# Kernel tuning notes

Hardware: AMD Instinct MI355X
Metric: run time of the kernel (lower is better)

## Reference

```python
import jax, jax.numpy as jnp
import numpy as np

B, N, C, H = 16, 1024, 768, 12
D = C // H          # head dim = 64
HID = 4 * C         # 3072
EPS = 1e-5


def layernorm(x, g, b):
    m = x.mean(-1, keepdims=True)
    v = ((x - m) ** 2).mean(-1, keepdims=True)
    return (x - m) * jax.lax.rsqrt(v + EPS) * g + b


def setup_inputs() -> dict:
    key = jax.random.key(0)
    ks = jax.random.split(key, 10)
    s = 0.02
    return {
        "x": jax.random.normal(ks[0], (B, N, C), dtype=jnp.float32),
        "ln1_g": jnp.ones((C,), jnp.float32), "ln1_b": jnp.zeros((C,), jnp.float32),
        "wq": jax.random.normal(ks[1], (C, C)) * s, "bq": jnp.zeros((C,), jnp.float32),
        "wk": jax.random.normal(ks[2], (C, C)) * s, "bk": jnp.zeros((C,), jnp.float32),
        "wv": jax.random.normal(ks[3], (C, C)) * s, "bv": jnp.zeros((C,), jnp.float32),
        "wp": jax.random.normal(ks[4], (C, C)) * s, "bp": jnp.zeros((C,), jnp.float32),
        "ln2_g": jnp.ones((C,), jnp.float32), "ln2_b": jnp.zeros((C,), jnp.float32),
        "w1": jax.random.normal(ks[5], (HID, C)) * s, "b1": jnp.zeros((HID,), jnp.float32),
        "w2": jax.random.normal(ks[6], (C, HID)) * s, "b2": jnp.zeros((C,), jnp.float32),
        "gate_h": jax.random.normal(ks[7], (H,), dtype=jnp.float32),
        "gate_f": jax.random.normal(ks[8], (HID,), dtype=jnp.float32),
    }


def reference(x, ln1_g, ln1_b, wq, bq, wk, bk, wv, bv, wp, bp,
              ln2_g, ln2_b, w1, b1, w2, b2, gate_h, gate_f):
    # steady-state path: k_dynamic=None, is_warmup=False -> dyn gates are all ones,
    # so head_mask / ffn_mask reduce to the hard static gates (STE is identity on ones).
    head_mask = (jax.nn.sigmoid(gate_h) > 0.5).astype(x.dtype)            # [H]
    hm = jnp.broadcast_to(head_mask, (B, H))                              # [B,H]

    # --- attention branch ---
    xn = layernorm(x, ln1_g, ln1_b)
    split = lambda t: t.reshape(B, N, H, D).transpose(0, 2, 1, 3)          # [B,H,N,D]
    q = split(xn @ wq.T + bq)
    k = split(xn @ wk.T + bk)
    v = split(xn @ wv.T + bv)
    scale = D ** -0.5
    attn = jax.nn.softmax(jnp.einsum('bhqd,bhkd->bhqk', q, k) * scale, axis=-1)
    y = jnp.einsum('bhqk,bhkd->bhqd', attn, v)
    y = y * hm[:, :, None, None]                                           # per-head mask on y
    xa = y.transpose(0, 2, 1, 3).reshape(B, N, C)
    hm_flat = jnp.repeat(hm, D, axis=-1).reshape(B, 1, C)                  # mask applied a 2nd time
    xa = (xa * hm_flat) @ wp.T + bp
    x = x + xa

    # --- gated MLP branch ---
    fmask = (jax.nn.sigmoid(gate_f) > 0.5).astype(x.dtype)[None, None, :]  # [1,1,HID]
    xn2 = layernorm(x, ln2_g, ln2_b)
    f1 = xn2 @ w1.T + b1
    f1 = jax.nn.gelu(f1 * fmask, approximate=False) * fmask                # mask -> GELU -> mask
    x = x + f1 @ w2.T + b2
    return x
```

## Files before the change

### kernel.cpp

```cpp
#include <hip/hip_runtime.h>

#define BB 16
#define NNN 1024
#define CC 768
#define HH 12
#define DD 64
#define HIDN 3072
#define ROWS (BB*NNN)

typedef _Float16 half8 __attribute__((ext_vector_type(8)));
typedef _Float16 half4 __attribute__((ext_vector_type(4)));
typedef float floatx4 __attribute__((ext_vector_type(4)));

#define GLOAD_LDS(g, l) __builtin_amdgcn_global_load_lds( \
    (const __attribute__((address_space(1))) void*)(g),    \
    (__attribute__((address_space(3))) void*)(l), 16, 0, 0)

#define RAW_BARRIER() do { asm volatile("" ::: "memory"); \
    __builtin_amdgcn_s_barrier(); asm volatile("" ::: "memory"); } while (0)
#define VMCNT_WAIT(n) __builtin_amdgcn_s_waitcnt((n) | 0x0F70)

__global__ void cvt_kernel(const float* __restrict__ src, _Float16* __restrict__ dst, int n4) {
    int i = blockIdx.x * blockDim.x + threadIdx.x;
    if (i < n4) {
        floatx4 v = ((const floatx4*)src)[i];
        half4 h;
        h[0] = (_Float16)v[0]; h[1] = (_Float16)v[1];
        h[2] = (_Float16)v[2]; h[3] = (_Float16)v[3];
        ((half4*)dst)[i] = h;
    }
}

__global__ __launch_bounds__(256) void scan_kernel(const float* __restrict__ gf,
                                                   const float* __restrict__ b1,
                                                   int* __restrict__ meta,
                                                   int* __restrict__ perm,
                                                   float* __restrict__ b1c) {
    int t = threadIdx.x;
    int base = t * 12;
    bool act[12];
    int cnt = 0;
    #pragma unroll
    for (int i = 0; i < 12; i++) { bool a = gf[base + i] > 0.0f; act[i] = a; cnt += a ? 1 : 0; }
    __shared__ int cs[256];
    __shared__ int tot;
    cs[t] = cnt;
    __syncthreads();
    if (t == 0) {
        int s = 0;
        for (int i = 0; i < 256; i++) { int c = cs[i]; cs[i] = s; s += c; }
        tot = s;
        meta[1] = s;
        meta[0] = (s + 127) & ~127;
    }
    __syncthreads();
    int off = cs[t];
    for (int i = t; i < HIDN; i += 256) { b1c[i] = 0.0f; perm[i] = -1; }
    __syncthreads();
    #pragma unroll
    for (int i = 0; i < 12; i++)
        if (act[i]) { perm[off] = base + i; b1c[off] = b1[base + i]; off++; }
    (void)tot;
}

__global__ void gatherW1_kernel(const float* __restrict__ src, const int* __restrict__ perm,
                                _Float16* __restrict__ dst) {
    int i = blockIdx.x * blockDim.x + threadIdx.x;
    int row = i / 192, c4 = i - row * 192;
    int s = perm[row];
    half4 h; h[0] = h[1] = h[2] = h[3] = (_Float16)0.0f;
    if (s >= 0) {
        floatx4 v = ((const floatx4*)(src + (size_t)s * CC))[c4];
        h[0] = (_Float16)v[0]; h[1] = (_Float16)v[1];
        h[2] = (_Float16)v[2]; h[3] = (_Float16)v[3];
    }
    ((half4*)dst)[i] = h;
}

__global__ void gatherW2_kernel(const float* __restrict__ src, const int* __restrict__ perm,
                                _Float16* __restrict__ dst) {
    int i = blockIdx.x * blockDim.x + threadIdx.x;
    int n = i / 768, j4 = (i - n * 768) * 4;
    const float* r = src + (size_t)n * HIDN;
    half4 h;
    #pragma unroll
    for (int e = 0; e < 4; e++) {
        int s = perm[j4 + e];
        h[e] = (s >= 0) ? (_Float16)r[s] : (_Float16)0.0f;
    }
    *(half4*)&dst[(size_t)n * HIDN + j4] = h;
}

__global__ __launch_bounds__(256) void ln_kernel(const float* __restrict__ x,
                                                 const float* __restrict__ g,
                                                 const float* __restrict__ b,
                                                 _Float16* __restrict__ out) {
    int row = blockIdx.x;
    int t = threadIdx.x;
    const float* xr = x + (size_t)row * CC;
    float v0 = xr[t], v1 = xr[t + 256], v2 = xr[t + 512];
    float s = v0 + v1 + v2;
    float q = v0 * v0 + v1 * v1 + v2 * v2;
    #pragma unroll
    for (int m = 1; m < 64; m <<= 1) {
        s += __shfl_xor(s, m, 64);
        q += __shfl_xor(q, m, 64);
    }
    __shared__ float red[8];
    int wv = t >> 6, lane = t & 63;
    if (lane == 0) { red[wv] = s; red[wv + 4] = q; }
    __syncthreads();
    s = red[0] + red[1] + red[2] + red[3];
    q = red[4] + red[5] + red[6] + red[7];
    float mean = s * (1.0f / CC);
    float var = q * (1.0f / CC) - mean * mean;
    float rs = rsqrtf(var + 1e-5f);
    _Float16* orow = out + (size_t)row * CC;
    orow[t]       = (_Float16)((v0 - mean) * rs * g[t]       + b[t]);
    orow[t + 256] = (_Float16)((v1 - mean) * rs * g[t + 256] + b[t + 256]);
    orow[t + 512] = (_Float16)((v2 - mean) * rs * g[t + 512] + b[t + 512]);
}

template <int MODE, int TM>
__global__ __launch_bounds__(256) void gemm_kernel(
    const _Float16* __restrict__ A,
    const _Float16* __restrict__ W,
    const float* __restrict__ bias0,
    const float* __restrict__ bias1,
    const float* __restrict__ bias2,
    const float* __restrict__ res,
    const float* __restrict__ gate,
    const float* __restrict__ hgate,
    void* __restrict__ out0,
    void* __restrict__ out1,
    void* __restrict__ out2,
    const int* __restrict__ meta,
    int M, int N, int K)
{
    constexpr int MI = TM / 32;
    constexpr int AISS = TM / 64;
    constexpr int NISS = AISS + 2;
    int GN = N >> 7, GM = M / TM;
    int f = blockIdx.x;
    int xcd = f & 7, slot = f >> 3;
    int m_idx = xcd * (GM >> 3) + slot / GN;
    int n_idx = slot - (slot / GN) * GN;
    int m0 = m_idx * TM, n0 = n_idx * 128;

    int Klen = K;
    if (meta) {
        if (MODE == 1) { if (n0 >= meta[0]) return; }
        if (MODE == 2) Klen = meta[0];
    }

    int seg = 0;
    if (MODE == 0) {
        seg = n0 / 768;
        int segc0 = n0 - seg * 768;
        int h0 = segc0 >> 6;
        if (hgate[h0] <= 0.0f && hgate[h0 + 1] <= 0.0f) return;
    }
    unsigned kmask = 0xFFFFFFFFu;
    if (MODE == 2 && hgate) {
        kmask = 0;
        for (int i = 0; i < HH; i++) kmask |= (hgate[i] > 0.0f ? 1u : 0u) << i;
    }

    __shared__ _Float16 As[3][TM * 32];
    __shared__ _Float16 Bs[3][128 * 32];
    int t = threadIdx.x;
    int lane = t & 63, w = t >> 6;
    int wm = (w >> 1) * (TM / 2), wn = (w & 1) * 64;
    int L = lane & 15, quad = lane >> 4;
    int rchunk = (quad ^ ((L >> 2) & 3)) * 8;

    floatx4 acc[MI][4];
    #pragma unroll
    for (int i = 0; i < MI; i++)
        #pragma unroll
        for (int j = 0; j < 4; j++)
            acc[i][j] = (floatx4){0.f, 0.f, 0.f, 0.f};

    const _Float16* agp[AISS];
    const _Float16* bgp[2];
    #pragma unroll
    for (int i = 0; i < AISS; i++) {
        int pc = i * 256 + t;
        int row = pc >> 2;
        int kc = (pc & 3) ^ ((pc >> 4) & 3);
        agp[i] = A + (size_t)(m0 + row) * K + kc * 8;
    }
    #pragma unroll
    for (int i = 0; i < 2; i++) {
        int pc = i * 256 + t;
        int row = pc >> 2;
        int kc = (pc & 3) ^ ((pc >> 4) & 3);
        bgp[i] = W + (size_t)(n0 + row) * K + kc * 8;
    }
    unsigned wb = (unsigned)w * 512;

    auto nextk = [&](int k0) -> int {
        if (MODE == 2)
            while (k0 < Klen && !((kmask >> ((k0 >> 6) & 31)) & 1)) k0 += 32;
        return k0;
    };
    auto stage = [&](int buf, int k0) {
        #pragma unroll
        for (int i = 0; i < AISS; i++) GLOAD_LDS(agp[i] + k0, &As[buf][i * 2048 + wb]);
        #pragma unroll
        for (int i = 0; i < 2; i++)    GLOAD_LDS(bgp[i] + k0, &Bs[buf][i * 2048 + wb]);
    };
    auto compute = [&](int buf) {
        half8 af[MI], bf[4];
        #pragma unroll
        for (int i = 0; i < MI; i++) af[i] = *(const half8*)&As[buf][(wm + i * 16 + L) * 32 + rchunk];
        #pragma unroll
        for (int j = 0; j < 4; j++)  bf[j] = *(const half8*)&Bs[buf][(wn + j * 16 + L) * 32 + rchunk];
        #pragma unroll
        for (int i = 0; i < MI; i++)
            #pragma unroll
            for (int j = 0; j < 4; j++)
                acc[i][j] = __builtin_amdgcn_mfma_f32_16x16x32_f16(af[i], bf[j], acc[i][j], 0, 0, 0);
    };

    int kcur = nextk(0);
    if (kcur < Klen) {
        stage(0, kcur);
        int kn1 = nextk(kcur + 32);
        int kn2 = Klen;
        if (kn1 < Klen) { stage(1, kn1); kn2 = nextk(kn1 + 32); }
        int buf = 0;
        while (kn2 < Klen) {
            int bnext = buf + 2; if (bnext >= 3) bnext -= 3;
            stage(bnext, kn2);
            VMCNT_WAIT(2 * NISS);
            RAW_BARRIER();
            compute(buf);
            RAW_BARRIER();
            buf = buf + 1; if (buf >= 3) buf -= 3;
            kcur = kn1; kn1 = kn2; kn2 = nextk(kn2 + 32);
        }
        if (kn1 < Klen) {
            VMCNT_WAIT(NISS);
            RAW_BARRIER();
            compute(buf);
            buf = buf + 1; if (buf >= 3) buf -= 3;
        }
        VMCNT_WAIT(0);
        RAW_BARRIER();
        compute(buf);
    }

    #pragma unroll
    for (int i = 0; i < MI; i++) {
        #pragma unroll
        for (int j = 0; j < 4; j++) {
            int gn = n0 + wn + j * 16 + L;
            if (MODE == 0) {
                int col = gn - seg * 768;
                const float* bsel = (seg == 0) ? bias0 : (seg == 1) ? bias1 : bias2;
                float bs = bsel[col];
                if (seg < 2) {
                    _Float16* o = (_Float16*)((seg == 0) ? out0 : out1);
                    #pragma unroll
                    for (int r = 0; r < 4; r++) {
                        int gm = m0 + wm + i * 16 + quad * 4 + r;
                        o[(size_t)gm * CC + col] = (_Float16)(acc[i][j][r] + bs);
                    }
                } else {
                    int gm0 = m0 + wm + i * 16 + quad * 4;
                    int b_ = gm0 >> 10, n_ = gm0 & 1023;
                    half4 pk;
                    #pragma unroll
                    for (int r = 0; r < 4; r++) pk[r] = (_Float16)(acc[i][j][r] + bs);
                    size_t idx = ((size_t)(b_ * HH + (col >> 6)) * 64 + (col & 63)) * NNN + n_;
                    *(half4*)&((_Float16*)out2)[idx] = pk;
                }
            } else {
                float bs = bias0[gn];
                #pragma unroll
                for (int r = 0; r < 4; r++) {
                    int gm = m0 + wm + i * 16 + quad * 4 + r;
                    float v = acc[i][j][r] + bs;
                    size_t idx = (size_t)gm * N + gn;
                    if (MODE == 1) {
                        float vv = 0.5f * v * (1.0f + erff(v * 0.70710678118f));
                        if (gate && !(gate[gn] > 0.0f)) vv = 0.0f;
                        ((_Float16*)out0)[idx] = (_Float16)vv;
                    } else {
                        ((float*)out0)[idx] = res[idx] + v;
                    }
                }
            }
        }
    }
}

__global__ __launch_bounds__(256) void attn_kernel(
    const _Float16* __restrict__ Q,
    const _Float16* __restrict__ Kp,
    const _Float16* __restrict__ Vt,
    const float* __restrict__ gate_h,
    _Float16* __restrict__ Y)
{
    int qt = blockIdx.x;
    int h  = blockIdx.y;
    int b  = blockIdx.z;
    int t = threadIdx.x;
    int q0 = qt * 64;
    size_t ybase = ((size_t)b * NNN + q0) * CC + h * DD;

    if (gate_h[h] <= 0.0f) {
        int r = t >> 2, c = (t & 3) * 16;
        half8 z = {(_Float16)0, (_Float16)0, (_Float16)0, (_Float16)0,
                   (_Float16)0, (_Float16)0, (_Float16)0, (_Float16)0};
        *(half8*)&Y[ybase + (size_t)r * CC + c]     = z;
        *(half8*)&Y[ybase + (size_t)r * CC + c + 8] = z;
        return;
    }

    __shared__ _Float16 Qs[64][72];
    __shared__ _Float16 Ks[64][72];
    __shared__ _Float16 Vs[64][72];
    __shared__ _Float16 Ps[64][72];

    int lane = t & 63, w = t >> 6;
    int L = lane & 15, quad = lane >> 4;

    {
        int r = t >> 2, c = (t & 3) * 16;
        const half8* src = (const half8*)(Q + ((size_t)b * NNN + q0 + r) * CC + h * DD + c);
        half8 h0 = src[0], h1 = src[1];
        #pragma unroll
        for (int e = 0; e < 8; e++) { h0[e] = h0[e] * (_Float16)0.125f; h1[e] = h1[e] * (_Float16)0.125f; }
        *(half8*)&Qs[r][c]     = h0;
        *(half8*)&Qs[r][c + 8] = h1;
    }

    floatx4 O[4];
    float m_[4], l_[4];
    #pragma unroll
    for (int i = 0; i < 4; i++) { O[i] = (floatx4){0.f,0.f,0.f,0.f}; m_[i] = -1e30f; l_[i] = 0.0f; }

    const size_t kbase = (size_t)b * NNN * CC + h * DD;
    const size_t vbase = (size_t)(b * HH + h) * DD * NNN;

    for (int kt = 0; kt < 16; ++kt) {
        int k0 = kt * 64;
        __syncthreads();
        {
            int r = t >> 2, c = (t & 3) * 16;
            const half8* ks = (const half8*)(Kp + kbase + (size_t)(k0 + r) * CC + c);
            half8 ka = ks[0], kb = ks[1];
            *(half8*)&Ks[r][c]     = ka;
            *(half8*)&Ks[r][c + 8] = kb;
            const half8* vs = (const half8*)(Vt + vbase + (size_t)r * NNN + k0 + c);
            half8 va = vs[0], vb = vs[1];
            *(half8*)&Vs[r][c]     = va;
            *(half8*)&Vs[r][c + 8] = vb;
        }
        __syncthreads();

        half8 aq0 = *(const half8*)&Qs[16 * w + L][quad * 8];
        half8 aq1 = *(const half8*)&Qs[16 * w + L][quad * 8 + 32];
        floatx4 s[4];
        #pragma unroll
        for (int j = 0; j < 4; j++) {
            half8 b0 = *(const half8*)&Ks[16 * j + L][quad * 8];
            half8 b1 = *(const half8*)&Ks[16 * j + L][quad * 8 + 32];
            floatx4 z = (floatx4){0.f,0.f,0.f,0.f};
            z = __builtin_amdgcn_mfma_f32_16x16x32_f16(aq0, b0, z, 0, 0, 0);
            z = __builtin_amdgcn_mfma_f32_16x16x32_f16(aq1, b1, z, 0, 0, 0);
            s[j] = z;
        }

        #pragma unroll
        for (int r = 0; r < 4; r++) {
            float mx = fmaxf(fmaxf(s[0][r], s[1][r]), fmaxf(s[2][r], s[3][r]));
            mx = fmaxf(mx, __shfl_xor(mx, 1, 64));
            mx = fmaxf(mx, __shfl_xor(mx, 2, 64));
            mx = fmaxf(mx, __shfl_xor(mx, 4, 64));
            mx = fmaxf(mx, __shfl_xor(mx, 8, 64));
            float mnew = fmaxf(m_[r], mx);
            float alpha = __expf(m_[r] - mnew);
            m_[r] = mnew;
            float ps = 0.0f;
            #pragma unroll
            for (int j = 0; j < 4; j++) {
                float p = __expf(s[j][r] - mnew);
                s[j][r] = p; ps += p;
                Ps[16 * w + quad * 4 + r][L + 16 * j] = (_Float16)p;
            }
            ps += __shfl_xor(ps, 1, 64);
            ps += __shfl_xor(ps, 2, 64);
            ps += __shfl_xor(ps, 4, 64);
            ps += __shfl_xor(ps, 8, 64);
            l_[r] = l_[r] * alpha + ps;
            #pragma unroll
            for (int t4 = 0; t4 < 4; t4++) O[t4][r] *= alpha;
        }
        __syncthreads();

        half8 ap0 = *(const half8*)&Ps[16 * w + L][quad * 8];
        half8 ap1 = *(const half8*)&Ps[16 * w + L][quad * 8 + 32];
        #pragma unroll
        for (int t4 = 0; t4 < 4; t4++) {
            half8 b0 = *(const half8*)&Vs[16 * t4 + L][quad * 8];
            half8 b1 = *(const half8*)&Vs[16 * t4 + L][quad * 8 + 32];
            O[t4] = __builtin_amdgcn_mfma_f32_16x16x32_f16(ap0, b0, O[t4], 0, 0, 0);
            O[t4] = __builtin_amdgcn_mfma_f32_16x16x32_f16(ap1, b1, O[t4], 0, 0, 0);
        }
    }

    __syncthreads();
    #pragma unroll
    for (int r = 0; r < 4; r++) {
        float inv = 1.0f / l_[r];
        #pragma unroll
        for (int t4 = 0; t4 < 4; t4++)
            Ps[16 * w + quad * 4 + r][16 * t4 + L] = (_Float16)(O[t4][r] * inv);
    }
    __syncthreads();
    {
        int r = t >> 2, c = (t & 3) * 16;
        half8 o0 = *(const half8*)&Ps[r][c];
        half8 o1 = *(const half8*)&Ps[r][c + 8];
        *(half8*)&Y[ybase + (size_t)r * CC + c]     = o0;
        *(half8*)&Y[ybase + (size_t)r * CC + c + 8] = o1;
    }
}

extern "C" void kernel_launch(void* const* d_in, const int* in_sizes, int n_in,
                              void* d_out, int out_size, void* d_ws, size_t ws_size,
                              hipStream_t stream)
{
    const float* x      = (const float*)d_in[0];
    const float* ln1_g  = (const float*)d_in[1];
    const float* ln1_b  = (const float*)d_in[2];
    const float* wq     = (const float*)d_in[3];
    const float* bq     = (const float*)d_in[4];
    const float* wk     = (const float*)d_in[5];
    const float* bk     = (const float*)d_in[6];
    const float* wv     = (const float*)d_in[7];
    const float* bv     = (const float*)d_in[8];
    const float* wp     = (const float*)d_in[9];
    const float* bp     = (const float*)d_in[10];
    const float* ln2_g  = (const float*)d_in[11];
    const float* ln2_b  = (const float*)d_in[12];
    const float* w1     = (const float*)d_in[13];
    const float* b1     = (const float*)d_in[14];
    const float* w2     = (const float*)d_in[15];
    const float* b2     = (const float*)d_in[16];
    const float* gate_h = (const float*)d_in[17];
    const float* gate_f = (const float*)d_in[18];

    char* ws = (char*)d_ws;
    _Float16* WQKVh = (_Float16*)(ws + 0);
    _Float16* WPh = (_Float16*)(ws + 3538944);
    _Float16* W1c = (_Float16*)(ws + 4718592);
    _Float16* W2c = (_Float16*)(ws + 9437184);
    _Float16* XN  = (_Float16*)(ws + 14155776);
    _Float16* Qb  = (_Float16*)(ws + 39321600);
    _Float16* Kb  = (_Float16*)(ws + 64487424);
    _Float16* Vtb = (_Float16*)(ws + 89653248);
    _Float16* Yb  = (_Float16*)(ws + 114819072);
    float*    X1  = (float*)   (ws + 139984896);
    _Float16* XN2 = (_Float16*)(ws + 114819072);
    _Float16* F1  = (_Float16*)(ws + 14155776);
    int*      meta = (int*)    (ws + 190316544);
    int*      perm = (int*)    (ws + 190316800);
    float*    b1c  = (float*)  (ws + 190329088);

    scan_kernel<<<1, 256, 0, stream>>>(gate_f, b1, meta, perm, b1c);

    cvt_kernel<<<576, 256, 0, stream>>>(wq, WQKVh, 147456);
    cvt_kernel<<<576, 256, 0, stream>>>(wk, WQKVh + 589824, 147456);
    cvt_kernel<<<576, 256, 0, stream>>>(wv, WQKVh + 1179648, 147456);
    cvt_kernel<<<576, 256, 0, stream>>>(wp, WPh, 147456);
    gatherW1_kernel<<<2304, 256, 0, stream>>>(w1, perm, W1c);
    gatherW2_kernel<<<2304, 256, 0, stream>>>(w2, perm, W2c);

    ln_kernel<<<ROWS, 256, 0, stream>>>(x, ln1_g, ln1_b, XN);

    gemm_kernel<0, 128><<<2304, 256, 0, stream>>>(
        XN, WQKVh, bq, bk, bv, nullptr, nullptr, gate_h, Qb, Kb, Vtb, nullptr, ROWS, 2304, CC);

    attn_kernel<<<dim3(16, HH, BB), 256, 0, stream>>>(Qb, Kb, Vtb, gate_h, Yb);

    gemm_kernel<2, 64><<<1536, 256, 0, stream>>>(
        Yb, WPh, bp, nullptr, nullptr, x, nullptr, gate_h, X1, nullptr, nullptr, nullptr, ROWS, CC, CC);

    ln_kernel<<<ROWS, 256, 0, stream>>>(X1, ln2_g, ln2_b, XN2);

    gemm_kernel<1, 128><<<3072, 256, 0, stream>>>(
        XN2, W1c, b1c, nullptr, nullptr, nullptr, nullptr, nullptr, F1, nullptr, nullptr, meta, ROWS, HIDN, CC);

    gemm_kernel<2, 128><<<768, 256, 0, stream>>>(
        F1, W2c, b2, nullptr, nullptr, X1, nullptr, nullptr, (float*)d_out, nullptr, nullptr, meta, ROWS, CC, HIDN);
}
```

Before: 515.8 us.

## Switch GEMM to BK=64 double-buffered pipeline with 8-chunk XOR swizzle

The GEMM kernel's K tile grows from 32 to 64, and the LDS pipeline drops from a triple buffer to a double buffer. LDS uses a new 8-way XOR swizzle, and each compute step runs two MFMA sub-steps. The next tile is staged only after the current one has been computed, which halves the barrier count per K but gives less load/compute overlap. The W2 GEMM also moves to TM=64 with twice the blocks, so more workgroups run on the long-K GEMM.

```diff
diff --git a/kernel.cpp b/kernel.cpp
--- a/kernel.cpp
+++ b/kernel.cpp
@@ -43,13 +43,11 @@
     #pragma unroll
     for (int i = 0; i < 12; i++) { bool a = gf[base + i] > 0.0f; act[i] = a; cnt += a ? 1 : 0; }
     __shared__ int cs[256];
-    __shared__ int tot;
     cs[t] = cnt;
     __syncthreads();
     if (t == 0) {
         int s = 0;
         for (int i = 0; i < 256; i++) { int c = cs[i]; cs[i] = s; s += c; }
-        tot = s;
         meta[1] = s;
         meta[0] = (s + 127) & ~127;
     }
@@ -60,7 +58,6 @@
     #pragma unroll
     for (int i = 0; i < 12; i++)
         if (act[i]) { perm[off] = base + i; b1c[off] = b1[base + i]; off++; }
-    (void)tot;
 }
 
 __global__ void gatherW1_kernel(const float* __restrict__ src, const int* __restrict__ perm,
@@ -138,8 +135,9 @@
     int M, int N, int K)
 {
     constexpr int MI = TM / 32;
-    constexpr int AISS = TM / 64;
-    constexpr int NISS = AISS + 2;
+    constexpr int AISS = TM / 32;
+    constexpr int BISS = 4;
+    constexpr int NISS = AISS + BISS;
     int GN = N >> 7, GM = M / TM;
     int f = blockIdx.x;
     int xcd = f & 7, slot = f >> 3;
@@ -166,13 +164,12 @@
         for (int i = 0; i < HH; i++) kmask |= (hgate[i] > 0.0f ? 1u : 0u) << i;
     }
 
-    __shared__ _Float16 As[3][TM * 32];
-    __shared__ _Float16 Bs[3][128 * 32];
+    __shared__ _Float16 As[2][TM * 64];
+    __shared__ _Float16 Bs[2][128 * 64];
     int t = threadIdx.x;
     int lane = t & 63, w = t >> 6;
     int wm = (w >> 1) * (TM / 2), wn = (w & 1) * 64;
     int L = lane & 15, quad = lane >> 4;
-    int rchunk = (quad ^ ((L >> 2) & 3)) * 8;
 
     floatx4 acc[MI][4];
     #pragma unroll
@@ -182,69 +179,73 @@
             acc[i][j] = (floatx4){0.f, 0.f, 0.f, 0.f};
 
     const _Float16* agp[AISS];
-    const _Float16* bgp[2];
+    const _Float16* bgp[BISS];
     #pragma unroll
     for (int i = 0; i < AISS; i++) {
         int pc = i * 256 + t;
-        int row = pc >> 2;
-        int kc = (pc & 3) ^ ((pc >> 4) & 3);
+        int row = pc >> 3;
+        int kc = (pc & 7) ^ (row & 7);
         agp[i] = A + (size_t)(m0 + row) * K + kc * 8;
     }
     #pragma unroll
-    for (int i = 0; i < 2; i++) {
+    for (int i = 0; i < BISS; i++) {
         int pc = i * 256 + t;
-        int row = pc >> 2;
-        int kc = (pc & 3) ^ ((pc >> 4) & 3);
+        int row = pc >> 3;
+        int kc = (pc & 7) ^ (row & 7);
         bgp[i] = W + (size_t)(n0 + row) * K + kc * 8;
     }
     unsigned wb = (unsigned)w * 512;
 
     auto nextk = [&](int k0) -> int {
         if (MODE == 2)
-            while (k0 < Klen && !((kmask >> ((k0 >> 6) & 31)) & 1)) k0 += 32;
+            while (k0 < Klen && !((kmask >> ((k0 >> 6) & 31)) & 1)) k0 += 64;
         return k0;
     };
     auto stage = [&](int buf, int k0) {
         #pragma unroll
         for (int i = 0; i < AISS; i++) GLOAD_LDS(agp[i] + k0, &As[buf][i * 2048 + wb]);
         #pragma unroll
-        for (int i = 0; i < 2; i++)    GLOAD_LDS(bgp[i] + k0, &Bs[buf][i * 2048 + wb]);
+        for (int i = 0; i < BISS; i++) GLOAD_LDS(bgp[i] + k0, &Bs[buf][i * 2048 + wb]);
     };
     auto compute = [&](int buf) {
-        half8 af[MI], bf[4];
-        #pragma unroll
-        for (int i = 0; i < MI; i++) af[i] = *(const half8*)&As[buf][(wm + i * 16 + L) * 32 + rchunk];
-        #pragma unroll
-        for (int j = 0; j < 4; j++)  bf[j] = *(const half8*)&Bs[buf][(wn + j * 16 + L) * 32 + rchunk];
-        #pragma unroll
-        for (int i = 0; i < MI; i++)
+        #pragma unroll
+        for (int kk = 0; kk < 2; kk++) {
+            half8 af[MI], bf[4];
+            #pragma unroll
+            for (int i = 0; i < MI; i++)
+                af[i] = *(const half8*)&As[buf][(wm + i * 16 + L) * 64 + ((kk * 4 + quad) ^ (L & 7)) * 8];
             #pragma unroll
             for (int j = 0; j < 4; j++)
-                acc[i][j] = __builtin_amdgcn_mfma_f32_16x16x32_f16(af[i], bf[j], acc[i][j], 0, 0, 0);
+                bf[j] = *(const half8*)&Bs[buf][(wn + j * 16 + L) * 64 + ((kk * 4 + quad) ^ (L & 7)) * 8];
+            #pragma unroll
+            for (int i = 0; i < MI; i++)
+                #pragma unroll
+                for (int j = 0; j < 4; j++)
+                    acc[i][j] = __builtin_amdgcn_mfma_f32_16x16x32_f16(af[i], bf[j], acc[i][j], 0, 0, 0);
+        }
     };
 
     int kcur = nextk(0);
     if (kcur < Klen) {
         stage(0, kcur);
-        int kn1 = nextk(kcur + 32);
+        int kn1 = nextk(kcur + 64);
         int kn2 = Klen;
-        if (kn1 < Klen) { stage(1, kn1); kn2 = nextk(kn1 + 32); }
+        if (kn1 < Klen) { stage(1, kn1); kn2 = nextk(kn1 + 64); }
         int buf = 0;
         while (kn2 < Klen) {
-            int bnext = buf + 2; if (bnext >= 3) bnext -= 3;
-            stage(bnext, kn2);
-            VMCNT_WAIT(2 * NISS);
+            VMCNT_WAIT(NISS);
             RAW_BARRIER();
             compute(buf);
             RAW_BARRIER();
-            buf = buf + 1; if (buf >= 3) buf -= 3;
-            kcur = kn1; kn1 = kn2; kn2 = nextk(kn2 + 32);
+            stage(buf, kn2);
+            buf ^= 1;
+            kn1 = kn2; kn2 = nextk(kn2 + 64);
         }
         if (kn1 < Klen) {
             VMCNT_WAIT(NISS);
             RAW_BARRIER();
             compute(buf);
-            buf = buf + 1; if (buf >= 3) buf -= 3;
+            buf ^= 1;
         }
         VMCNT_WAIT(0);
         RAW_BARRIER();
@@ -495,6 +496,6 @@
     gemm_kernel<1, 128><<<3072, 256, 0, stream>>>(
         XN2, W1c, b1c, nullptr, nullptr, nullptr, nullptr, nullptr, F1, nullptr, nullptr, meta, ROWS, HIDN, CC);
 
-    gemm_kernel<2, 128><<<768, 256, 0, stream>>>(
+    gemm_kernel<2, 64><<<1536, 256, 0, stream>>>(
         F1, W2c, b2, nullptr, nullptr, X1, nullptr, nullptr, (float*)d_out, nullptr, nullptr, meta, ROWS, CC, HIDN);
 }
```

Measured after the change: 465.3 us. 1.11x faster.
